# Performance work log

Hardware: AMD Instinct MI355X
Metric: run time of the kernel (lower is better)

Reference implementation:

```python
import jax, jax.numpy as jnp
import numpy as np

N_NODES = 50000


def _gine(x, src, dst, edge_embed, lin_w, lin_b, nn_w, nn_b):
    # PyG GINEConv (eps=0): out = nn(x + sum_{j->i} ReLU(x_j + lin(edge_attr)))
    e = edge_embed @ lin_w + lin_b              # [E, d_in]
    msg = jax.nn.relu(x[src] + e)               # gather + fuse, [E, d_in]
    agg = jax.ops.segment_sum(msg, dst, num_segments=N_NODES)  # scatter-add, [N, d_in]
    return (x + agg) @ nn_w + nn_b              # small MLP, [N, d_out]


def setup_inputs() -> dict:
    key = jax.random.key(0)
    ks = jax.random.split(key, 20)
    E = 800000
    h = 128
    sc = lambda f_in: 1.0 / np.sqrt(f_in)
    inp = {
        "x": jax.random.normal(ks[0], (N_NODES, 1), jnp.float32),
        "edge_index": jax.random.randint(ks[1], (2, E), 0, N_NODES, jnp.int64),
        "edge_attr": jax.random.normal(ks[2], (E, 1), jnp.float32),
        "em_w": jax.random.normal(ks[3], (1, h), jnp.float32) * sc(1),
        "em_b": jnp.zeros((h,), jnp.float32),
        "l1_w": jax.random.normal(ks[4], (h, 1), jnp.float32) * sc(h),
        "l1_b": jnp.zeros((1,), jnp.float32),
        "n1_w": jax.random.normal(ks[5], (1, h), jnp.float32) * sc(1),
        "n1_b": jnp.zeros((h,), jnp.float32),
        "l2_w": jax.random.normal(ks[6], (h, h), jnp.float32) * sc(h),
        "l2_b": jnp.zeros((h,), jnp.float32),
        "n2_w": jax.random.normal(ks[7], (h, h), jnp.float32) * sc(h),
        "n2_b": jnp.zeros((h,), jnp.float32),
        "l3_w": jax.random.normal(ks[8], (h, h), jnp.float32) * sc(h),
        "l3_b": jnp.zeros((h,), jnp.float32),
        "n3_w": jax.random.normal(ks[9], (h, h), jnp.float32) * sc(h),
        "n3_b": jnp.zeros((h,), jnp.float32),
        "dec_w": jax.random.normal(ks[10], (2 * h, 1), jnp.float32) * sc(2 * h),
        "dec_b": jnp.zeros((1,), jnp.float32),
    }
    return inp


def reference(x, edge_index, edge_attr, em_w, em_b, l1_w, l1_b, n1_w, n1_b,
              l2_w, l2_b, n2_w, n2_b, l3_w, l3_b, n3_w, n3_b, dec_w, dec_b):
    src, dst = edge_index[0], edge_index[1]
    edge_embed = edge_attr @ em_w + em_b                      # [E, 128]
    hdn = _gine(x,   src, dst, edge_embed, l1_w, l1_b, n1_w, n1_b)
    hdn = _gine(hdn, src, dst, edge_embed, l2_w, l2_b, n2_w, n2_b)
    hdn = _gine(hdn, src, dst, edge_embed, l3_w, l3_b, n3_w, n3_b)
    h_cat = jnp.concatenate([hdn[src], hdn[dst]], axis=-1)    # [E, 256]
    return h_cat @ dec_w + dec_b                              # [E, 1]
```

## Files before the change

### kernel.cpp

```cpp
#include <hip/hip_runtime.h>

#define H 128
#define CAPC 3072


typedef unsigned long long ull;
using bf16x8 = __attribute__((ext_vector_type(8))) short;
using f32x4  = __attribute__((ext_vector_type(4))) float;

__device__ __forceinline__ float bf2f(unsigned short v) {
  return __uint_as_float(((unsigned)v) << 16);
}
__device__ __forceinline__ unsigned short bf16r(float v) {
  unsigned u = __float_as_uint(v);
  u = (u + 0x7FFFu + ((u >> 16) & 1u)) >> 16;
  return (unsigned short)u;
}
__device__ __forceinline__ unsigned bf16pair(float a, float b) {
  return (unsigned)bf16r(a) | ((unsigned)bf16r(b) << 16);
}

__global__ __launch_bounds__(256) void init_consts(
    const float* __restrict__ em_w, const float* __restrict__ em_b,
    const float* __restrict__ l1_w, const float* __restrict__ l1_b,
    const float* __restrict__ l2_w, const float* __restrict__ l2_b,
    const float* __restrict__ n1_b,
    const float* __restrict__ l3_w, const float* __restrict__ l3_b,
    const float* __restrict__ n2w, const float* __restrict__ n3w,
    const float* __restrict__ n3b, const float* __restrict__ dec_w,
    float* __restrict__ consts, int* __restrict__ cursor,
    unsigned short* __restrict__ w2t) {
  if (blockIdx.x > 0) {
    const int i = (blockIdx.x - 1) * 256 + threadIdx.x;
    if (i < H * H) {
      const int j = i >> 7, k = i & (H - 1);
      w2t[k * H + j] = bf16r(n2w[i]);
    }
    return;
  }
  const int k = threadIdx.x;
  cursor[k] = 0;
  cursor[k + 256] = 0;
  __shared__ float sa[H], sc[H];
  if (k < H) {
    float u2 = 0.f, c2 = 0.f, u3 = 0.f, c3 = 0.f, vA = 0.f, vB = 0.f;
    for (int j = 0; j < H; ++j) {
      const float ew = em_w[j], eb = em_b[j];
      u2 = fmaf(ew, l2_w[j * H + k], u2);
      c2 = fmaf(eb, l2_w[j * H + k], c2);
      u3 = fmaf(ew, l3_w[j * H + k], u3);
      c3 = fmaf(eb, l3_w[j * H + k], c3);
      vA = fmaf(n3w[k * H + j], dec_w[j], vA);
      vB = fmaf(n3w[k * H + j], dec_w[H + j], vB);
    }
    consts[2 + k]         = u2;
    consts[2 + H + k]     = c2 + l2_b[k] + n1_b[k];
    consts[2 + 2 * H + k] = u3;
    consts[2 + 3 * H + k] = c3 + l3_b[k];
    consts[514 + k]       = vA;
    consts[642 + k]       = vB;
    sa[k] = em_w[k] * l1_w[k];
    sc[k] = em_b[k] * l1_w[k];
  }
  __syncthreads();
  for (int s = 64; s > 0; s >>= 1) {
    if (k < s) { sa[k] += sa[k + s]; sc[k] += sc[k + s]; }
    __syncthreads();
  }
  if (k == 0) { consts[0] = sa[0]; consts[1] = sc[0] + l1_b[0]; }
  __syncthreads();
  if (k < H) {
    sa[k] = n3b[k] * dec_w[k];
    sc[k] = n3b[k] * dec_w[H + k];
  }
  __syncthreads();
  for (int s = 64; s > 0; s >>= 1) {
    if (k < s) { sa[k] += sa[k + s]; sc[k] += sc[k + s]; }
    __syncthreads();
  }
  if (k == 0) { consts[770] = sa[0]; consts[771] = sc[0]; }
}

__global__ __launch_bounds__(1024) void bin_scatter(
    const int* __restrict__ src, const int* __restrict__ dst,
    const float* __restrict__ ea, int* __restrict__ cursor,
    ull* __restrict__ spc, int E, int NBUCK) {
  __shared__ int lhist[512];
  __shared__ int lbase[512];
  const int tid = threadIdx.x;
  const int base = blockIdx.x * 2048 + tid * 2;
  if (tid < 512) lhist[tid] = 0;
  __syncthreads();
  int s_[2], d_[2], b_[2], r_[2];
  float a_[2];
#pragma unroll
  for (int j = 0; j < 2; ++j) {
    const int e = base + j;
    if (e < E) {
      s_[j] = src[e]; d_[j] = dst[e]; a_[j] = ea[e];
      b_[j] = d_[j] >> 7;
      r_[j] = atomicAdd(&lhist[b_[j]], 1);
    } else {
      b_[j] = -1;
    }
  }
  __syncthreads();
  if (tid < NBUCK && lhist[tid] > 0)
    lbase[tid] = atomicAdd(&cursor[tid], lhist[tid]);
  __syncthreads();
#pragma unroll
  for (int j = 0; j < 2; ++j) {
    if (b_[j] >= 0) {
      const int pl = lbase[b_[j]] + r_[j];
      if (pl < CAPC)
        spc[(size_t)b_[j] * CAPC + pl] =
            ((ull)(unsigned)(s_[j] | ((d_[j] & 127) << 16)) << 32) |
            (ull)(unsigned)__float_as_uint(a_[j]);
    }
  }
}

__global__ __launch_bounds__(1024) void fine_scatter(
    const int* __restrict__ cursor, const ull* __restrict__ spc,
    const float* __restrict__ x, const float* __restrict__ consts,
    int2* __restrict__ spf, int* __restrict__ rowstart,
    float* __restrict__ s1, int N) {
  __shared__ int lh[128];
  __shared__ int sd[128];
  __shared__ int cur[128];
  __shared__ int2 pay[CAPC];
  const int tid = threadIdx.x;
  const int b = blockIdx.x;
  const int cnt = min(cursor[b], CAPC);
  const size_t rbase = (size_t)b * CAPC;
  if (tid < 128) lh[tid] = 0;
  __syncthreads();
  for (int i = tid; i < cnt; i += 1024)
    atomicAdd(&lh[(int)((spc[rbase + i] >> 48) & 127u)], 1);
  __syncthreads();
  if (tid < 128) sd[tid] = lh[tid];
  __syncthreads();
  for (int off = 1; off < 128; off <<= 1) {
    int t = 0;
    if (tid < 128 && tid >= off) t = sd[tid - off];
    __syncthreads();
    if (tid < 128) sd[tid] += t;
    __syncthreads();
  }
  if (tid < 128) {
    const int ex = sd[tid] - lh[tid];
    cur[tid] = ex;
    rowstart[b * 129 + tid] = (int)rbase + ex;
    if (tid == 0) rowstart[b * 129 + 128] = (int)rbase + cnt;
  }
  __syncthreads();
  for (int i = tid; i < cnt; i += 1024) {
    const ull payv = spc[rbase + i];
    const int dl = (int)((payv >> 48) & 127u);
    const int pos = atomicAdd(&cur[dl], 1);
    pay[pos] = make_int2((int)((payv >> 32) & 0xFFFFu), (int)(unsigned)payv);
  }
  __syncthreads();
  for (int i = tid; i < cnt; i += 1024) spf[rbase + i] = pay[i];
  const int lane = tid & 63, w = tid >> 6;
  const float a1 = consts[0], c1 = consts[1];
  for (int i = w; i < 128; i += 16) {
    const int n = (b << 7) + i;
    if (n >= N) break;
    const int rsl = sd[i] - lh[i], ci = lh[i];
    float part = 0.f;
    for (int j = lane; j < ci; j += 64) {
      const int2 pv = pay[rsl + j];
      part += fmaxf(x[pv.x] + fmaf(a1, __int_as_float(pv.y), c1), 0.f);
    }
#pragma unroll
    for (int o = 32; o >= 1; o >>= 1) part += __shfl_xor(part, o, 64);
    if (lane == 0) s1[n] = x[n] + part;
  }
}

__global__ __launch_bounds__(1024) void layer2_fused(
    const int* __restrict__ rowstart, const int2* __restrict__ sp,
    const float* __restrict__ s1, const float* __restrict__ n1w,
    const float* __restrict__ n1b, const float* __restrict__ consts,
    const unsigned short* __restrict__ w2t, const float* __restrict__ n2b,
    unsigned short* __restrict__ h2b, int N) {
  __shared__ unsigned short t2s[16][136];
  __shared__ unsigned short hs[16][128];
  const int tid = threadIdx.x, w = tid >> 6, lane = tid & 63;
  const int node0 = blockIdx.x * 16;
  {
    const int n = node0 + w;
    if (n < N) {
      const int rb = (n >> 7) * 129 + (n & 127);
      const int rs = rowstart[rb], re = rowstart[rb + 1];
      const float w0 = n1w[lane],            w1 = n1w[lane + 64];
      const float u0 = consts[2 + lane],     u1 = consts[2 + lane + 64];
      const float c0 = consts[2 + H + lane], c1 = consts[2 + H + lane + 64];
      float acc0 = 0.f, acc1 = 0.f;
      for (int base = rs; base < re; base += 64) {
        const int i = base + lane;
        float s1v = 0.f, eav = 0.f;
        if (i < re) {
          const int2 sv = sp[i];
          s1v = s1[sv.x];
          eav = __int_as_float(sv.y);
        }
        const int cntv = min(64, re - base);
        for (int j = 0; j < cntv; ++j) {
          const float s = __shfl(s1v, j, 64);
          const float a = __shfl(eav, j, 64);
          acc0 += fmaxf(fmaf(s, w0, fmaf(a, u0, c0)), 0.f);
          acc1 += fmaxf(fmaf(s, w1, fmaf(a, u1, c1)), 0.f);
        }
      }
      const float sn = s1[n];
      t2s[w][lane]      = bf16r(fmaf(sn, w0, n1b[lane])      + acc0);
      t2s[w][lane + 64] = bf16r(fmaf(sn, w1, n1b[lane + 64]) + acc1);
    } else {
      t2s[w][lane] = 0;
      t2s[w][lane + 64] = 0;
    }
  }
  __syncthreads();
  if (w < 8) {
    const int t = w, col = lane & 15, quad = lane >> 4;
    const bf16x8 a0 = *(const bf16x8*)&t2s[col][quad * 8];
    const bf16x8 a1 = *(const bf16x8*)&t2s[col][32 + quad * 8];
    const bf16x8 a2 = *(const bf16x8*)&t2s[col][64 + quad * 8];
    const bf16x8 a3 = *(const bf16x8*)&t2s[col][96 + quad * 8];
    const bf16x8* bcol =
        (const bf16x8*)(w2t + (size_t)(t * 16 + col) * H + quad * 8);
    f32x4 acc = {0.f, 0.f, 0.f, 0.f};
    acc = __builtin_amdgcn_mfma_f32_16x16x32_bf16(a0, bcol[0], acc, 0, 0, 0);
    acc = __builtin_amdgcn_mfma_f32_16x16x32_bf16(a1, bcol[4], acc, 0, 0, 0);
    acc = __builtin_amdgcn_mfma_f32_16x16x32_bf16(a2, bcol[8], acc, 0, 0, 0);
    acc = __builtin_amdgcn_mfma_f32_16x16x32_bf16(a3, bcol[12], acc, 0, 0, 0);
    const float bias = n2b[t * 16 + col];
#pragma unroll
    for (int r = 0; r < 4; ++r)
      hs[quad * 4 + r][t * 16 + col] = bf16r(acc[r] + bias);
  }
  __syncthreads();
  const int row = tid >> 6, word = tid & 63;
  ((unsigned*)h2b)[(size_t)(node0 + row) * 64 + word] =
      ((const unsigned*)hs)[row * 64 + word];
}

__global__ __launch_bounds__(256) void layer3_dot(
    const int* __restrict__ rowstart, const int2* __restrict__ sp,
    const unsigned short* __restrict__ h2b, const float* __restrict__ consts,
    float* __restrict__ p, float* __restrict__ q, int N) {
  const int n = (blockIdx.x * blockDim.x + threadIdx.x) >> 6;
  const int lane = threadIdx.x & 63;
  if (n >= N) return;
  const int k0 = 2 * lane;
  const float u0 = consts[2 + 2 * H + k0], u1 = consts[2 + 2 * H + k0 + 1];
  const float c0 = consts[2 + 3 * H + k0], c1 = consts[2 + 3 * H + k0 + 1];
  const float vA0 = consts[514 + k0], vA1 = consts[514 + k0 + 1];
  const float vB0 = consts[642 + k0], vB1 = consts[642 + k0 + 1];
  const int rb = (n >> 7) * 129 + (n & 127);
  const int rs = rowstart[rb], re = rowstart[rb + 1];
  float acc0 = 0.f, acc1 = 0.f;
  for (int base = rs; base < re; base += 64) {
    const int i = base + lane;
    int esrc = 0;
    float eav = 0.f;
    if (i < re) {
      const int2 sv = sp[i];
      esrc = sv.x;
      eav = __int_as_float(sv.y);
    }
    const int cntv = min(64, re - base);
    int j = 0;
    for (; j + 4 <= cntv; j += 4) {
      const int s0 = __shfl(esrc, j, 64),     s1i = __shfl(esrc, j + 1, 64);
      const int s2 = __shfl(esrc, j + 2, 64), s3 = __shfl(esrc, j + 3, 64);
      const float a0 = __shfl(eav, j, 64),     a1 = __shfl(eav, j + 1, 64);
      const float a2 = __shfl(eav, j + 2, 64), a3 = __shfl(eav, j + 3, 64);
      const ushort2 h0 = *(const ushort2*)&h2b[(size_t)s0 * H + k0];
      const ushort2 h1 = *(const ushort2*)&h2b[(size_t)s1i * H + k0];
      const ushort2 h2v = *(const ushort2*)&h2b[(size_t)s2 * H + k0];
      const ushort2 h3 = *(const ushort2*)&h2b[(size_t)s3 * H + k0];
      acc0 += fmaxf(bf2f(h0.x) + fmaf(a0, u0, c0), 0.f);
      acc1 += fmaxf(bf2f(h0.y) + fmaf(a0, u1, c1), 0.f);
      acc0 += fmaxf(bf2f(h1.x) + fmaf(a1, u0, c0), 0.f);
      acc1 += fmaxf(bf2f(h1.y) + fmaf(a1, u1, c1), 0.f);
      acc0 += fmaxf(bf2f(h2v.x) + fmaf(a2, u0, c0), 0.f);
      acc1 += fmaxf(bf2f(h2v.y) + fmaf(a2, u1, c1), 0.f);
      acc0 += fmaxf(bf2f(h3.x) + fmaf(a3, u0, c0), 0.f);
      acc1 += fmaxf(bf2f(h3.y) + fmaf(a3, u1, c1), 0.f);
    }
    for (; j < cntv; ++j) {
      const int s0 = __shfl(esrc, j, 64);
      const float a0 = __shfl(eav, j, 64);
      const ushort2 hv = *(const ushort2*)&h2b[(size_t)s0 * H + k0];
      acc0 += fmaxf(bf2f(hv.x) + fmaf(a0, u0, c0), 0.f);
      acc1 += fmaxf(bf2f(hv.y) + fmaf(a0, u1, c1), 0.f);
    }
  }
  const ushort2 hn = *(const ushort2*)&h2b[(size_t)n * H + k0];
  const float t0 = bf2f(hn.x) + acc0;
  const float t1 = bf2f(hn.y) + acc1;
  float pd = t0 * vA0 + t1 * vA1;
  float qd = t0 * vB0 + t1 * vB1;
#pragma unroll
  for (int o = 32; o >= 1; o >>= 1) {
    pd += __shfl_xor(pd, o, 64);
    qd += __shfl_xor(qd, o, 64);
  }
  if (lane == 0) {
    p[n] = pd + consts[770];
    q[n] = qd + consts[771];
  }
}

__global__ void final_kernel(const int* __restrict__ src,
                             const int* __restrict__ dst,
                             const float* __restrict__ p,
                             const float* __restrict__ q,
                             const float* __restrict__ dec_b,
                             float* __restrict__ out, int E) {
  const int e = blockIdx.x * blockDim.x + threadIdx.x;
  if (e < E) out[e] = p[src[e]] + q[dst[e]] + dec_b[0];
}

extern "C" void kernel_launch(void* const* d_in, const int* in_sizes, int n_in,
                              void* d_out, int out_size, void* d_ws, size_t ws_size,
                              hipStream_t stream) {
  const float* x     = (const float*)d_in[0];
  const int*   ei    = (const int*)d_in[1];
  const float* ea    = (const float*)d_in[2];
  const float* em_w  = (const float*)d_in[3];
  const float* em_b  = (const float*)d_in[4];
  const float* l1_w  = (const float*)d_in[5];
  const float* l1_b  = (const float*)d_in[6];
  const float* n1_w  = (const float*)d_in[7];
  const float* n1_b  = (const float*)d_in[8];
  const float* l2_w  = (const float*)d_in[9];
  const float* l2_b  = (const float*)d_in[10];
  const float* n2_w  = (const float*)d_in[11];
  const float* n2_b  = (const float*)d_in[12];
  const float* l3_w  = (const float*)d_in[13];
  const float* l3_b  = (const float*)d_in[14];
  const float* n3_w  = (const float*)d_in[15];
  const float* n3_b  = (const float*)d_in[16];
  const float* dec_w = (const float*)d_in[17];
  const float* dec_b = (const float*)d_in[18];
  float* out = (float*)d_out;

  const int N = in_sizes[0];
  const int E = in_sizes[2];
  const int* src = ei;
  const int* dst = ei + E;

  const int NBUCK  = (N + 127) >> 7;
  const int NBATCH = (E + 2047) >> 11;
  const int NPAD   = ((N + 15) / 16) * 16;
  const int NT16   = NPAD / 16;

  float* ws       = (float*)d_ws;
  float* consts   = ws;
  ull*   spc      = (ull*)(ws + 1024);
  int2*  spf      = (int2*)(spc + (size_t)NBUCK * CAPC);
  unsigned short* h2b = (unsigned short*)(spf + (size_t)NBUCK * CAPC);
  unsigned short* w2t = h2b + (size_t)NPAD * H;
  float* s1       = (float*)(w2t + H * H);
  float* p        = s1 + N;
  float* q        = p + N;
  int*   cursor   = (int*)(q + N);
  int*   rowstart = cursor + 512;

  init_consts<<<65, 256, 0, stream>>>(em_w, em_b, l1_w, l1_b, l2_w, l2_b,
                                      n1_b, l3_w, l3_b, n2_w, n3_w, n3_b,
                                      dec_w, consts, cursor, w2t);
  bin_scatter<<<NBATCH, 1024, 0, stream>>>(src, dst, ea, cursor, spc, E, NBUCK);
  fine_scatter<<<NBUCK, 1024, 0, stream>>>(cursor, spc, x, consts, spf,
                                           rowstart, s1, N);
  layer2_fused<<<NT16, 1024, 0, stream>>>(rowstart, spf, s1, n1_w, n1_b,
                                          consts, w2t, n2_b, h2b, N);
  layer3_dot<<<(N + 3) / 4, 256, 0, stream>>>(rowstart, spf, h2b, consts,
                                              p, q, N);
  final_kernel<<<(E + 255) / 256, 256, 0, stream>>>(src, dst, p, q, dec_b, out, E);
}
```

Before: 219.4 us.

## Restructure layer2 so each wave owns a 16-node tile without block barriers

The layer-2 kernel now has each 64-lane wave aggregate 16 nodes in sequence and then run the full 16x128 MFMA tile itself. Previously 16 waves each aggregated one node, then 8 waves did the matmul behind block-wide __syncthreads. Wave barriers replace block barriers, so load imbalance between waves no longer stalls the block, and all waves share the MFMA work. In exchange, per-wave latency for the aggregation grows, since each wave processes its 16 nodes serially. It also adds register pressure from holding 32 accumulator values per lane.

```diff
diff --git a/kernel.cpp b/kernel.cpp
--- a/kernel.cpp
+++ b/kernel.cpp
@@ -179,56 +179,60 @@
   }
 }
 
-__global__ __launch_bounds__(1024) void layer2_fused(
+__global__ __launch_bounds__(256) void layer2_wave(
     const int* __restrict__ rowstart, const int2* __restrict__ sp,
     const float* __restrict__ s1, const float* __restrict__ n1w,
     const float* __restrict__ n1b, const float* __restrict__ consts,
     const unsigned short* __restrict__ w2t, const float* __restrict__ n2b,
     unsigned short* __restrict__ h2b, int N) {
-  __shared__ unsigned short t2s[16][136];
-  __shared__ unsigned short hs[16][128];
+  __shared__ unsigned short t2s[4][16][136];
   const int tid = threadIdx.x, w = tid >> 6, lane = tid & 63;
-  const int node0 = blockIdx.x * 16;
+  const int node0 = (blockIdx.x * 4 + w) * 16;
   {
-    const int n = node0 + w;
-    if (n < N) {
-      const int rb = (n >> 7) * 129 + (n & 127);
-      const int rs = rowstart[rb], re = rowstart[rb + 1];
-      const float w0 = n1w[lane],            w1 = n1w[lane + 64];
-      const float u0 = consts[2 + lane],     u1 = consts[2 + lane + 64];
-      const float c0 = consts[2 + H + lane], c1 = consts[2 + H + lane + 64];
-      float acc0 = 0.f, acc1 = 0.f;
-      for (int base = rs; base < re; base += 64) {
-        const int i = base + lane;
-        float s1v = 0.f, eav = 0.f;
-        if (i < re) {
-          const int2 sv = sp[i];
-          s1v = s1[sv.x];
-          eav = __int_as_float(sv.y);
+    const float w0 = n1w[lane],            w1 = n1w[lane + 64];
+    const float u0 = consts[2 + lane],     u1 = consts[2 + lane + 64];
+    const float c0 = consts[2 + H + lane], c1 = consts[2 + H + lane + 64];
+    const float b0 = n1b[lane],            b1 = n1b[lane + 64];
+    for (int m = 0; m < 16; ++m) {
+      const int n = node0 + m;
+      if (n < N) {
+        const int rb = (n >> 7) * 129 + (n & 127);
+        const int rs = rowstart[rb], re = rowstart[rb + 1];
+        float acc0 = 0.f, acc1 = 0.f;
+        for (int base = rs; base < re; base += 64) {
+          const int i = base + lane;
+          float s1v = 0.f, eav = 0.f;
+          if (i < re) {
+            const int2 sv = sp[i];
+            s1v = s1[sv.x];
+            eav = __int_as_float(sv.y);
+          }
+          const int cntv = min(64, re - base);
+          for (int j = 0; j < cntv; ++j) {
+            const float s = __shfl(s1v, j, 64);
+            const float a = __shfl(eav, j, 64);
+            acc0 += fmaxf(fmaf(s, w0, fmaf(a, u0, c0)), 0.f);
+            acc1 += fmaxf(fmaf(s, w1, fmaf(a, u1, c1)), 0.f);
+          }
         }
-        const int cntv = min(64, re - base);
-        for (int j = 0; j < cntv; ++j) {
-          const float s = __shfl(s1v, j, 64);
-          const float a = __shfl(eav, j, 64);
-          acc0 += fmaxf(fmaf(s, w0, fmaf(a, u0, c0)), 0.f);
-          acc1 += fmaxf(fmaf(s, w1, fmaf(a, u1, c1)), 0.f);
-        }
+        const float sn = s1[n];
+        t2s[w][m][lane]      = bf16r(fmaf(sn, w0, b0) + acc0);
+        t2s[w][m][lane + 64] = bf16r(fmaf(sn, w1, b1) + acc1);
+      } else {
+        t2s[w][m][lane] = 0;
+        t2s[w][m][lane + 64] = 0;
       }
-      const float sn = s1[n];
-      t2s[w][lane]      = bf16r(fmaf(sn, w0, n1b[lane])      + acc0);
-      t2s[w][lane + 64] = bf16r(fmaf(sn, w1, n1b[lane + 64]) + acc1);
-    } else {
-      t2s[w][lane] = 0;
-      t2s[w][lane + 64] = 0;
-    }
-  }
-  __syncthreads();
-  if (w < 8) {
-    const int t = w, col = lane & 15, quad = lane >> 4;
-    const bf16x8 a0 = *(const bf16x8*)&t2s[col][quad * 8];
-    const bf16x8 a1 = *(const bf16x8*)&t2s[col][32 + quad * 8];
-    const bf16x8 a2 = *(const bf16x8*)&t2s[col][64 + quad * 8];
-    const bf16x8 a3 = *(const bf16x8*)&t2s[col][96 + quad * 8];
+    }
+  }
+  __builtin_amdgcn_wave_barrier();
+  const int col = lane & 15, quad = lane >> 4;
+  const bf16x8 a0 = *(const bf16x8*)&t2s[w][col][quad * 8];
+  const bf16x8 a1 = *(const bf16x8*)&t2s[w][col][32 + quad * 8];
+  const bf16x8 a2 = *(const bf16x8*)&t2s[w][col][64 + quad * 8];
+  const bf16x8 a3 = *(const bf16x8*)&t2s[w][col][96 + quad * 8];
+  float hv[8][4];
+#pragma unroll
+  for (int t = 0; t < 8; ++t) {
     const bf16x8* bcol =
         (const bf16x8*)(w2t + (size_t)(t * 16 + col) * H + quad * 8);
     f32x4 acc = {0.f, 0.f, 0.f, 0.f};
@@ -238,13 +242,22 @@
     acc = __builtin_amdgcn_mfma_f32_16x16x32_bf16(a3, bcol[12], acc, 0, 0, 0);
     const float bias = n2b[t * 16 + col];
 #pragma unroll
+    for (int r = 0; r < 4; ++r) hv[t][r] = acc[r] + bias;
+  }
+  __builtin_amdgcn_wave_barrier();
+#pragma unroll
+  for (int t = 0; t < 8; ++t)
+#pragma unroll
     for (int r = 0; r < 4; ++r)
-      hs[quad * 4 + r][t * 16 + col] = bf16r(acc[r] + bias);
-  }
-  __syncthreads();
-  const int row = tid >> 6, word = tid & 63;
-  ((unsigned*)h2b)[(size_t)(node0 + row) * 64 + word] =
-      ((const unsigned*)hs)[row * 64 + word];
+      t2s[w][quad * 4 + r][t * 16 + col] = bf16r(hv[t][r]);
+  __builtin_amdgcn_wave_barrier();
+#pragma unroll
+  for (int m = 0; m < 16; ++m) {
+    const int n = node0 + m;
+    if (n < N)
+      ((unsigned*)h2b)[(size_t)n * 64 + lane] =
+          *(const unsigned*)&t2s[w][m][2 * lane];
+  }
 }
 
 __global__ __launch_bounds__(256) void layer3_dot(
@@ -357,7 +370,7 @@
   const int NBUCK  = (N + 127) >> 7;
   const int NBATCH = (E + 2047) >> 11;
   const int NPAD   = ((N + 15) / 16) * 16;
-  const int NT16   = NPAD / 16;
+  const int NB64   = (N + 63) / 64;
 
   float* ws       = (float*)d_ws;
   float* consts   = ws;
@@ -377,8 +390,8 @@
   bin_scatter<<<NBATCH, 1024, 0, stream>>>(src, dst, ea, cursor, spc, E, NBUCK);
   fine_scatter<<<NBUCK, 1024, 0, stream>>>(cursor, spc, x, consts, spf,
                                            rowstart, s1, N);
-  layer2_fused<<<NT16, 1024, 0, stream>>>(rowstart, spf, s1, n1_w, n1_b,
-                                          consts, w2t, n2_b, h2b, N);
+  layer2_wave<<<NB64, 256, 0, stream>>>(rowstart, spf, s1, n1_w, n1_b,
+                                        consts, w2t, n2_b, h2b, N);
   layer3_dot<<<(N + 3) / 4, 256, 0, stream>>>(rowstart, spf, h2b, consts,
                                               p, q, N);
   final_kernel<<<(E + 255) / 256, 256, 0, stream>>>(src, dst, p, q, dec_b, out, E);
```

Result: slower. 228.5 us (+4.1%).
